# Optimization experiments

Measured on AMD Instinct MI355X. Metric: run time of the kernel, lower is better.

The kernel has to match this reference:

```python
import jax, jax.numpy as jnp
import numpy as np

EPS = 1e-8  # torch F.cosine_similarity default eps


def setup_inputs() -> dict:
    key = jax.random.key(0)
    k1, k2, k3 = jax.random.split(key, 3)
    B, D, C = 65536, 512, 10000
    embeddings = jax.random.normal(k1, (B, D), dtype=jnp.float32)
    labels = jax.random.randint(k2, (B,), 0, C, dtype=jnp.int64)
    prototypes = jax.random.normal(k3, (C, D), dtype=jnp.float32)
    return {"embeddings": embeddings, "labels": labels, "prototypes": prototypes}


def reference(embeddings, labels, prototypes):
    # Batched gather of per-sample prototypes: [B, D]
    protos = prototypes[labels]
    # Cosine similarity per sample (torch eps semantics: clamp norm at eps)
    e_norm = jnp.maximum(jnp.linalg.norm(embeddings, axis=-1), EPS)
    p_norm = jnp.maximum(jnp.linalg.norm(protos, axis=-1), EPS)
    cos = jnp.sum(embeddings * protos, axis=-1) / (e_norm * p_norm)
    return 1.0 - jnp.mean(cos)
```

## Files before the change

### kernel.cpp

```cpp
#include <hip/hip_runtime.h>
#include <math.h>

#define COS_EPS 1e-8f

__global__ __launch_bounds__(256) void assignment_loss_kernel(
    const float* __restrict__ emb,
    const int*   __restrict__ labels,
    const float* __restrict__ protos,
    float*       __restrict__ acc,
    int B, int D)
{
    const int lane           = threadIdx.x & 63;
    const int wave_in_block  = threadIdx.x >> 6;
    const int waves_per_blk  = blockDim.x >> 6;
    const int global_wave    = blockIdx.x * waves_per_blk + wave_in_block;
    const int n_waves        = gridDim.x * waves_per_blk;
    const int nchunks        = D >> 8;

    float local = 0.0f;

    for (int s = global_wave; s < B; s += n_waves) {
        const int lbl = labels[s];
        const float4* __restrict__ e =
            (const float4*)(emb + (size_t)s * (size_t)D);
        const float4* __restrict__ p =
            (const float4*)(protos + (size_t)lbl * (size_t)D);

        float dot = 0.0f, esq = 0.0f, psq = 0.0f;
        #pragma unroll
        for (int c = 0; c < 2; ++c) {
            if (c < nchunks) {
                float4 ev = e[c * 64 + lane];
                float4 pv = p[c * 64 + lane];
                dot = fmaf(ev.x, pv.x, fmaf(ev.y, pv.y, fmaf(ev.z, pv.z, fmaf(ev.w, pv.w, dot))));
                esq = fmaf(ev.x, ev.x, fmaf(ev.y, ev.y, fmaf(ev.z, ev.z, fmaf(ev.w, ev.w, esq))));
                psq = fmaf(pv.x, pv.x, fmaf(pv.y, pv.y, fmaf(pv.z, pv.z, fmaf(pv.w, pv.w, psq))));
            }
        }
        for (int c = 2; c < nchunks; ++c) {
            float4 ev = e[c * 64 + lane];
            float4 pv = p[c * 64 + lane];
            dot = fmaf(ev.x, pv.x, fmaf(ev.y, pv.y, fmaf(ev.z, pv.z, fmaf(ev.w, pv.w, dot))));
            esq = fmaf(ev.x, ev.x, fmaf(ev.y, ev.y, fmaf(ev.z, ev.z, fmaf(ev.w, ev.w, esq))));
            psq = fmaf(pv.x, pv.x, fmaf(pv.y, pv.y, fmaf(pv.z, pv.z, fmaf(pv.w, pv.w, psq))));
        }

        #pragma unroll
        for (int off = 32; off > 0; off >>= 1) {
            dot += __shfl_xor(dot, off, 64);
            esq += __shfl_xor(esq, off, 64);
            psq += __shfl_xor(psq, off, 64);
        }

        if (lane == 0) {
            float en = fmaxf(sqrtf(esq), COS_EPS);
            float pn = fmaxf(sqrtf(psq), COS_EPS);
            local += dot / (en * pn);
        }
    }

    __shared__ float smem[8];
    if (lane == 0) smem[wave_in_block] = local;
    __syncthreads();
    if (threadIdx.x == 0) {
        float bs = 0.0f;
        for (int w = 0; w < waves_per_blk; ++w) bs += smem[w];
        atomicAdd(acc, bs);
    }
}

__global__ void assignment_loss_finalize(const float* __restrict__ acc,
                                         float* __restrict__ out,
                                         float invB)
{
    out[0] = 1.0f - acc[0] * invB;
}

extern "C" void kernel_launch(void* const* d_in, const int* in_sizes, int n_in,
                              void* d_out, int out_size, void* d_ws, size_t ws_size,
                              hipStream_t stream) {
    const float* emb    = (const float*)d_in[0];
    const int*   labels = (const int*)  d_in[1];
    const float* protos = (const float*)d_in[2];
    float*       out    = (float*)d_out;
    float*       acc    = (float*)d_ws;

    const int B = in_sizes[1];
    const int D = in_sizes[0] / B;

    hipMemsetAsync(acc, 0, sizeof(float), stream);

    const int block = 256;
    const int grid  = 1024;
    assignment_loss_kernel<<<grid, block, 0, stream>>>(emb, labels, protos, acc, B, D);
    assignment_loss_finalize<<<1, 1, 0, stream>>>(acc, out, 1.0f / (float)B);
}
```

Measured before the change: 215.2 us.

## Map one sample per thread instead of one sample per wave

Assigns each thread a full 512-dim sample, looping over float4 chunks serially. This removes the per-sample cross-lane shuffle reductions, leaving one wave reduction at the end, and shrinks the grid to 256 blocks. The cost is that adjacent lanes now read rows 2KB apart, so global loads are no longer coalesced and memory efficiency may fall sharply.

```diff
diff --git a/kernel.cpp b/kernel.cpp
--- a/kernel.cpp
+++ b/kernel.cpp
@@ -2,6 +2,12 @@
 #include <math.h>
 
 #define COS_EPS 1e-8f
+
+typedef float vfloat4 __attribute__((ext_vector_type(4)));
+
+__device__ __forceinline__ float dot4(vfloat4 a, vfloat4 b) {
+    return fmaf(a.x, b.x, fmaf(a.y, b.y, fmaf(a.z, b.z, a.w * b.w)));
+}
 
 __global__ __launch_bounds__(256) void assignment_loss_kernel(
     const float* __restrict__ emb,
@@ -10,61 +16,63 @@
     float*       __restrict__ acc,
     int B, int D)
 {
-    const int lane           = threadIdx.x & 63;
-    const int wave_in_block  = threadIdx.x >> 6;
-    const int waves_per_blk  = blockDim.x >> 6;
-    const int global_wave    = blockIdx.x * waves_per_blk + wave_in_block;
-    const int n_waves        = gridDim.x * waves_per_blk;
-    const int nchunks        = D >> 8;
+    const int tid     = blockIdx.x * blockDim.x + threadIdx.x;
+    const int nthread = gridDim.x * blockDim.x;
+    const int lane    = threadIdx.x & 63;
+    const int wib     = threadIdx.x >> 6;
+    const int wpb     = blockDim.x >> 6;
 
     float local = 0.0f;
 
-    for (int s = global_wave; s < B; s += n_waves) {
-        const int lbl = labels[s];
-        const float4* __restrict__ e =
-            (const float4*)(emb + (size_t)s * (size_t)D);
-        const float4* __restrict__ p =
-            (const float4*)(protos + (size_t)lbl * (size_t)D);
+    if (D == 512) {
+        for (int s = tid; s < B; s += nthread) {
+            const int lbl = labels[s];
+            const vfloat4* __restrict__ e = (const vfloat4*)(emb    + (size_t)s   * 512);
+            const vfloat4* __restrict__ p = (const vfloat4*)(protos + (size_t)lbl * 512);
 
-        float dot = 0.0f, esq = 0.0f, psq = 0.0f;
-        #pragma unroll
-        for (int c = 0; c < 2; ++c) {
-            if (c < nchunks) {
-                float4 ev = e[c * 64 + lane];
-                float4 pv = p[c * 64 + lane];
-                dot = fmaf(ev.x, pv.x, fmaf(ev.y, pv.y, fmaf(ev.z, pv.z, fmaf(ev.w, pv.w, dot))));
-                esq = fmaf(ev.x, ev.x, fmaf(ev.y, ev.y, fmaf(ev.z, ev.z, fmaf(ev.w, ev.w, esq))));
-                psq = fmaf(pv.x, pv.x, fmaf(pv.y, pv.y, fmaf(pv.z, pv.z, fmaf(pv.w, pv.w, psq))));
+            float dot = 0.f, esq = 0.f, psq = 0.f;
+            #pragma unroll 8
+            for (int c = 0; c < 128; ++c) {
+                vfloat4 ev = e[c];
+                vfloat4 pv = p[c];
+                dot += dot4(ev, pv);
+                esq += dot4(ev, ev);
+                psq += dot4(pv, pv);
             }
+
+            float en = fmaxf(sqrtf(esq), COS_EPS);
+            float pn = fmaxf(sqrtf(psq), COS_EPS);
+            local += dot / (en * pn);
         }
-        for (int c = 2; c < nchunks; ++c) {
-            float4 ev = e[c * 64 + lane];
-            float4 pv = p[c * 64 + lane];
-            dot = fmaf(ev.x, pv.x, fmaf(ev.y, pv.y, fmaf(ev.z, pv.z, fmaf(ev.w, pv.w, dot))));
-            esq = fmaf(ev.x, ev.x, fmaf(ev.y, ev.y, fmaf(ev.z, ev.z, fmaf(ev.w, ev.w, esq))));
-            psq = fmaf(pv.x, pv.x, fmaf(pv.y, pv.y, fmaf(pv.z, pv.z, fmaf(pv.w, pv.w, psq))));
-        }
-
-        #pragma unroll
-        for (int off = 32; off > 0; off >>= 1) {
-            dot += __shfl_xor(dot, off, 64);
-            esq += __shfl_xor(esq, off, 64);
-            psq += __shfl_xor(psq, off, 64);
-        }
-
-        if (lane == 0) {
+    } else {
+        const int nchunks = D >> 2;
+        for (int s = tid; s < B; s += nthread) {
+            const int lbl = labels[s];
+            const vfloat4* e = (const vfloat4*)(emb    + (size_t)s   * (size_t)D);
+            const vfloat4* p = (const vfloat4*)(protos + (size_t)lbl * (size_t)D);
+            float dot = 0.f, esq = 0.f, psq = 0.f;
+            for (int c = 0; c < nchunks; ++c) {
+                vfloat4 ev = e[c];
+                vfloat4 pv = p[c];
+                dot += dot4(ev, pv);
+                esq += dot4(ev, ev);
+                psq += dot4(pv, pv);
+            }
             float en = fmaxf(sqrtf(esq), COS_EPS);
             float pn = fmaxf(sqrtf(psq), COS_EPS);
             local += dot / (en * pn);
         }
     }
 
+    #pragma unroll
+    for (int off = 32; off > 0; off >>= 1) local += __shfl_xor(local, off, 64);
+
     __shared__ float smem[8];
-    if (lane == 0) smem[wave_in_block] = local;
+    if (lane == 0) smem[wib] = local;
     __syncthreads();
     if (threadIdx.x == 0) {
         float bs = 0.0f;
-        for (int w = 0; w < waves_per_blk; ++w) bs += smem[w];
+        for (int w = 0; w < wpb; ++w) bs += smem[w];
         atomicAdd(acc, bs);
     }
 }
@@ -91,7 +99,7 @@
     hipMemsetAsync(acc, 0, sizeof(float), stream);
 
     const int block = 256;
-    const int grid  = 1024;
-    assignment_loss_kernel<<<grid, block, 0, stream>>>(emb, labels, protos, acc, B, D);
+    const int grid  = 512;
+    assignment_loss_kernel<<<256, block, 0, stream>>>(emb, labels, protos, acc, B, D);
     assignment_loss_finalize<<<1, 1, 0, stream>>>(acc, out, 1.0f / (float)B);
 }
```

New measurement: 231.1 us. 1.07x slower.
